# Performance work log

Hardware: AMD Instinct MI355X
Metric: run time of the kernel (lower is better)

## Reference

```python
import jax, jax.numpy as jnp
import numpy as np

B, DP, N = 8, 3, 2048
DM, K = 128, 20
C4 = DM // 4


def _gather(pts, idx):
    # pts: (b, n, c), idx: (b, n, k) -> (b, n, k, c)
    return jax.vmap(lambda p, i: p[i])(pts, idx)


def _bn(x, gamma, beta, eps=1e-5):
    # train-mode BatchNorm1d; x: (b, c, n), stats over (batch, points)
    mu = jnp.mean(x, axis=(0, 2), keepdims=True)
    var = jnp.var(x, axis=(0, 2), keepdims=True)
    return gamma[None, :, None] * (x - mu) * jax.lax.rsqrt(var + eps) + beta[None, :, None]


def setup_inputs() -> dict:
    key = jax.random.key(0)
    ks = iter(jax.random.split(key, 32))

    def U(shape):
        s = 1.0 / np.sqrt(shape[-1])
        return jax.random.uniform(next(ks), shape, jnp.float32, -s, s)

    d = {}
    d['features'] = jax.random.normal(next(ks), (B, DP, N), jnp.float32)
    d['fc1_w'] = U((DM, DP)); d['fc1_b'] = U((DM,))
    d['fc2_w'] = U((DM, DM)); d['fc2_b'] = U((DM,))
    d['bn_g'] = jnp.ones((DM,), jnp.float32); d['bn_b'] = jnp.zeros((DM,), jnp.float32)
    d['fb1_w'] = U((DM, 2 * DP)); d['fb1_b'] = U((DM,))
    d['fb2_w'] = U((DM, DM)); d['fb2_b'] = U((DM,))
    d['fg1_w'] = U((DM, DM)); d['fg1_b'] = U((DM,))
    d['fg2_w'] = U((DM, DM)); d['fg2_b'] = U((DM,))
    d['wq'] = U((DM, DM)); d['wk'] = U((DM, DM)); d['wv'] = U((DM, DM))
    d['sa_qk_w'] = U((C4, DM))  # q_conv and k_conv share this weight
    d['sa_v_w'] = U((DM, DM)); d['sa_v_b'] = U((DM,))
    d['sa_t_w'] = U((DM, DM)); d['sa_t_b'] = U((DM,))
    d['sa_bn_g'] = jnp.ones((DM,), jnp.float32); d['sa_bn_b'] = jnp.zeros((DM,), jnp.float32)
    return d


def reference(features, fc1_w, fc1_b, fc2_w, fc2_b, bn_g, bn_b,
              fb1_w, fb1_b, fb2_w, fb2_b, fg1_w, fg1_b, fg2_w, fg2_b,
              wq, wk, wv, sa_qk_w, sa_v_w, sa_v_b, sa_t_w, sa_t_b,
              sa_bn_g, sa_bn_b):
    x = features  # (b, dp, n)
    # --- kNN: negative squared pairwise distance, top-k largest = nearest ---
    inner = -2.0 * jnp.einsum('bdn,bdm->bnm', x, x)
    xx = jnp.sum(x * x, axis=1)  # (b, n)
    pd = -xx[:, :, None] - inner - xx[:, None, :]  # (b, n, n)
    idx = jax.lax.top_k(pd, K)[1]  # (b, n, K) neighbor indices
    # --- get_graph_feature: gather neighbors, concat (nbr - ctr, ctr) ---
    xt = jnp.transpose(x, (0, 2, 1))  # (b, n, dp)
    nbr = _gather(xt, idx)  # (b, n, K, dp)
    ctr = jnp.broadcast_to(xt[:, :, None, :], nbr.shape)
    kf = jnp.concatenate([nbr - ctr, ctr], axis=-1)  # (b, n, K, 2*dp)
    # fb edge MLP
    kf = jax.nn.relu(kf @ fb1_w.T + fb1_b) @ fb2_w.T + fb2_b  # (b, n, K, DM)
    # --- point-transformer attention ---
    x1 = xt @ fc1_w.T + fc1_b  # (b, n, DM)
    q = x1 @ wq.T
    kg = _gather(x1 @ wk.T, idx)  # (b, n, K, DM)
    vg = _gather(x1 @ wv.T, idx)  # (b, n, K, DM)
    a = q[:, :, None, :] - kg + kf
    a = jax.nn.relu(a @ fg1_w.T + fg1_b) @ fg2_w.T + fg2_b  # fc_gamma
    attn = jax.nn.log_softmax(a / jnp.sqrt(jnp.float32(DM)), axis=-2)  # over K
    res = jnp.einsum('bnkf,bnkf->bnf', attn, vg + kf)  # (b, n, DM)
    res = jnp.transpose(res @ fc2_w.T + fc2_b, (0, 2, 1))  # (b, DM, n)
    res = jax.nn.relu(_bn(res, bn_g, bn_b)) + jnp.transpose(x1, (0, 2, 1))
    # --- SA_Layer: offset self-attention (q and k share weights) ---
    xqk = jnp.einsum('cd,bdn->bcn', sa_qk_w, res)  # (b, C4, n)
    energy = jnp.einsum('bcn,bcm->bnm', xqk, xqk)  # (b, n, n)
    att = jax.nn.softmax(energy, axis=-1)
    att = att / (1e-9 + jnp.sum(att, axis=1, keepdims=True))
    xv = jnp.einsum('cd,bdn->bcn', sa_v_w, res) + sa_v_b[None, :, None]
    xr = jnp.einsum('bcn,bnm->bcm', xv, att)  # x_v @ attention
    xr = jnp.einsum('cd,bdn->bcn', sa_t_w, res - xr) + sa_t_b[None, :, None]
    xr = jax.nn.relu(_bn(xr, sa_bn_g, sa_bn_b))
    out = res + xr  # (b, DM, n)
    return (jnp.transpose(out, (0, 2, 1)), attn)
```

## Files before the change

### kernel.cpp

```cpp
#include <hip/hip_runtime.h>

#define NPTS 16384
#define NB 2048
#define KNN 20

typedef __attribute__((ext_vector_type(4))) float f32x4;
typedef __attribute__((ext_vector_type(8))) short short8;

union U4S8 { uint4 q; short8 s; };
union W4   { unsigned u[4]; short8 s; };

__device__ __forceinline__ unsigned bf16_rne(float v){
    unsigned u = __float_as_uint(v);
    return (u + 0x7fffu + ((u>>16)&1u)) >> 16;
}
__device__ __forceinline__ unsigned pack_hl(float v){
    unsigned hi = bf16_rne(v);
    float r = v - __uint_as_float(hi<<16);
    unsigned lo = bf16_rne(r);
    return hi | (lo<<16);
}
__device__ __forceinline__ void split_hl(uint4 w0, uint4 w1, short8& hi, short8& lo){
    W4 h, l;
    h.u[0] = __builtin_amdgcn_perm(w0.y, w0.x, 0x05040100u);
    l.u[0] = __builtin_amdgcn_perm(w0.y, w0.x, 0x07060302u);
    h.u[1] = __builtin_amdgcn_perm(w0.w, w0.z, 0x05040100u);
    l.u[1] = __builtin_amdgcn_perm(w0.w, w0.z, 0x07060302u);
    h.u[2] = __builtin_amdgcn_perm(w1.y, w1.x, 0x05040100u);
    l.u[2] = __builtin_amdgcn_perm(w1.y, w1.x, 0x07060302u);
    h.u[3] = __builtin_amdgcn_perm(w1.w, w1.z, 0x05040100u);
    l.u[3] = __builtin_amdgcn_perm(w1.w, w1.z, 0x07060302u);
    hi = h.s; lo = l.s;
}
__device__ __forceinline__ f32x4 e3_mfma(short8 Ah, short8 Al, short8 Bh, short8 Bl){
    f32x4 acc = (f32x4){0.f,0.f,0.f,0.f};
    acc = __builtin_amdgcn_mfma_f32_16x16x32_bf16(Al, Bh, acc, 0,0,0);
    acc = __builtin_amdgcn_mfma_f32_16x16x32_bf16(Ah, Bl, acc, 0,0,0);
    acc = __builtin_amdgcn_mfma_f32_16x16x32_bf16(Ah, Bh, acc, 0,0,0);
    return acc;
}

__global__ void transpose_kernel(const float* in, float* out, int C){
    int gid = blockIdx.x*256 + threadIdx.x;
    if (gid >= 128*C) return;
    int j = gid / C, c = gid - j*C;
    out[gid] = in[c*128 + j];
}

__global__ void pack_bfrag_kernel(const float* w0, const float* w1, const float* w2, unsigned short* out){
    int gid = blockIdx.x*256 + threadIdx.x;
    if (gid >= 3*16384) return;
    int m = gid >> 14, r = gid & 16383;
    const float* W = (m==0)?w0:(m==1)?w1:w2;
    int e = r & 7, lane = (r>>3) & 63, ks = (r>>9)&3, ct = r>>11;
    int c = ct*16 + (lane&15), j = ks*32 + (lane>>4)*8 + e;
    out[gid] = (unsigned short)bf16_rne(W[c*128 + j]);
}

__global__ __launch_bounds__(256) void knn_kernel(const float* feat, int* g_idx){
    __shared__ float sx[2048], sy[2048], sz[2048];
    __shared__ int swin[32*20];
    int tid = threadIdx.x;
    int p0 = blockIdx.x * 32;
    int b = p0 >> 11;
    const float* fb = feat + b*3*2048;
    for (int i = tid; i < 2048; i += 256){ sx[i]=fb[i]; sy[i]=fb[2048+i]; sz[i]=fb[4096+i]; }
    __syncthreads();

    int chunk = tid & 7, pl = tid >> 3;
    int n = (p0 + pl) & 2047;
    double xi = sx[n], yi = sy[n], zi = sz[n];

    const double SENT = __longlong_as_double(0x7FE0000000000000ll);
    double val[20];
#pragma unroll
    for (int k=0;k<20;k++) val[k] = SENT;

    int base = chunk*256;
    for (int ii=0; ii<256; ii++){
        int i = (ii + (chunk<<2)) & 255;
        int j = base + i;
        double dx = (double)sx[j]-xi, dy = (double)sy[j]-yi, dz = (double)sz[j]-zi;
        double d2 = dx*dx + dy*dy + dz*dz;
        long long kb = ((__double_as_longlong(d2) & ~2047ll) | (long long)j) + (1ll<<61);
        double key = __longlong_as_double(kb);
#pragma unroll
        for (int s=19; s>=1; s--)
            val[s] = fmax(val[s-1], fmin(val[s], key));
        val[0] = fmin(val[0], key);
    }

    for (int kk=0; kk<20; kk++){
        double h = val[0];
        h = fmin(h, __shfl_xor(h, 1));
        h = fmin(h, __shfl_xor(h, 2));
        h = fmin(h, __shfl_xor(h, 4));
        if (val[0] == h){
            swin[pl*20 + kk] = (int)(__double_as_longlong(h) & 2047ll);
#pragma unroll
            for (int s=0;s<19;s++) val[s] = val[s+1];
            val[19] = SENT;
        }
    }
    __syncthreads();
    for (int t = tid; t < 640; t += 256)
        g_idx[p0*20 + t] = swin[t];
}

__global__ void x1_kernel(const float* feat, const float* w, const float* bias, float* x1){
    int gid = blockIdx.x*256 + threadIdx.x;
    int p = gid >> 7, c = gid & 127;
    int b = p >> 11, n = p & 2047;
    const float* fb = feat + b*6144 + n;
    float v = bias[c];
    v += w[c*3+0]*fb[0];
    v += w[c*3+1]*fb[2048];
    v += w[c*3+2]*fb[4096];
    x1[gid] = v;
}

__global__ __launch_bounds__(256) void qkv_kernel(const float* x1, const float* wqT, const float* wkT,
                                                  const float* wvT, float* q, float* k1, float* v1){
    __shared__ float sx[16][128];
    int tid = threadIdx.x;
    int p0 = blockIdx.x * 16;
    for (int t = tid; t < 2048; t += 256) sx[t>>7][t&127] = x1[p0*128 + t];
    __syncthreads();
    int cg = tid & 31, pg = tid >> 5, c0 = cg*4;
    float aq[2][4] = {{0,0,0,0},{0,0,0,0}};
    float ak[2][4] = {{0,0,0,0},{0,0,0,0}};
    float av[2][4] = {{0,0,0,0},{0,0,0,0}};
    for (int j=0;j<128;j++){
        float xa = sx[pg][j], xb = sx[pg+8][j];
        float4 wq4 = *(const float4*)&wqT[j*128 + c0];
        float4 wk4 = *(const float4*)&wkT[j*128 + c0];
        float4 wv4 = *(const float4*)&wvT[j*128 + c0];
        const float* wqp = &wq4.x; const float* wkp = &wk4.x; const float* wvp = &wv4.x;
#pragma unroll
        for (int ci=0; ci<4; ci++){
            aq[0][ci] += wqp[ci]*xa; aq[1][ci] += wqp[ci]*xb;
            ak[0][ci] += wkp[ci]*xa; ak[1][ci] += wkp[ci]*xb;
            av[0][ci] += wvp[ci]*xa; av[1][ci] += wvp[ci]*xb;
        }
    }
#pragma unroll
    for (int pp=0; pp<2; pp++){
        int p = p0 + pg + pp*8;
        *(float4*)&q [p*128 + c0] = make_float4(aq[pp][0],aq[pp][1],aq[pp][2],aq[pp][3]);
        *(float4*)&k1[p*128 + c0] = make_float4(ak[pp][0],ak[pp][1],ak[pp][2],ak[pp][3]);
        *(float4*)&v1[p*128 + c0] = make_float4(av[pp][0],av[pp][1],av[pp][2],av[pp][3]);
    }
}

__device__ __forceinline__ void stage_gemm(const unsigned* buf, const unsigned short* wb,
                                           int lane, int ct0, f32x4 acc[5][2]){
    short8 bf[2][4];
#pragma unroll
    for (int ci=0; ci<2; ci++)
#pragma unroll
    for (int ks=0; ks<4; ks++){
        U4S8 u; u.q = *(const uint4*)(wb + ((ct0+ci)*4 + ks)*512 + lane*8);
        bf[ci][ks] = u.s;
    }
#pragma unroll
    for (int rt=0; rt<5; rt++)
#pragma unroll
    for (int ci=0; ci<2; ci++)
        acc[rt][ci] = (f32x4){0.f,0.f,0.f,0.f};
    int abase = (lane&15)*132 + (lane>>4)*8;
#pragma unroll
    for (int rt=0; rt<5; rt++){
#pragma unroll
        for (int ks=0; ks<4; ks++){
            const unsigned* ap = buf + rt*16*132 + ks*32 + abase;
            uint4 w0 = *(const uint4*)ap;
            uint4 w1 = *(const uint4*)(ap+4);
            short8 hi, lo;
            split_hl(w0, w1, hi, lo);
#pragma unroll
            for (int ci=0; ci<2; ci++){
                acc[rt][ci] = __builtin_amdgcn_mfma_f32_16x16x32_bf16(hi, bf[ci][ks], acc[rt][ci], 0,0,0);
                acc[rt][ci] = __builtin_amdgcn_mfma_f32_16x16x32_bf16(lo, bf[ci][ks], acc[rt][ci], 0,0,0);
            }
        }
    }
}

__global__ __launch_bounds__(256, 3) void attn_kernel(
        const float* feat, const int* g_idx, const float* g_q, const float* g_k1, const float* g_v1,
        const unsigned short* wpk,
        const float* fb1w, const float* fb1b, const float* fb2b, const float* fg1b, const float* fg2b,
        float* g_attn, float* g_res){
    __shared__ __align__(16) unsigned buf[80*132];
    __shared__ float sh_q[512];
    __shared__ float sh_e[80*6];
    __shared__ int   sh_ix[80];
    int tid = threadIdx.x;
    int lane = tid & 63, wave = tid >> 6;
    int gp0 = blockIdx.x * 4;
    int b = gp0 >> 11;
    size_t kvbase = (size_t)b*2048*128;

    sh_q[tid]     = g_q[gp0*128 + tid];
    sh_q[tid+256] = g_q[gp0*128 + tid + 256];
    if (tid < 80){
        int r = tid;
        int nb = g_idx[gp0*20 + r];
        sh_ix[r] = nb;
        int p = (r*205) >> 12;
        int n = (gp0 & 2047) + p;
        const float* fbp = feat + b*6144;
        float cx = fbp[n], cy = fbp[2048+n], cz = fbp[4096+n];
        float nx = fbp[nb], ny = fbp[2048+nb], nz = fbp[4096+nb];
        sh_e[r*6+0] = nx-cx; sh_e[r*6+1] = ny-cy; sh_e[r*6+2] = nz-cz;
        sh_e[r*6+3] = cx;    sh_e[r*6+4] = cy;    sh_e[r*6+5] = cz;
    }
    __syncthreads();

    {
        int c = tid & 127, rh = tid >> 7;
        float w0=fb1w[c*6+0], w1=fb1w[c*6+1], w2=fb1w[c*6+2], w3=fb1w[c*6+3], w4=fb1w[c*6+4], w5=fb1w[c*6+5];
        float bb = fb1b[c];
#pragma unroll
        for (int rr=0; rr<40; rr++){
            int r = rr*2 + rh;
            const float* e = &sh_e[r*6];
            float v = bb + w0*e[0]+w1*e[1]+w2*e[2]+w3*e[3]+w4*e[4]+w5*e[5];
            buf[r*132 + c] = pack_hl(fmaxf(v, 0.f));
        }
    }
    __syncthreads();

    int ct0 = wave*2;
    int colA = ct0*16 + (lane&15);
    int colB = colA + 16;
    int quad = lane >> 4;
    f32x4 acc[5][2];

    stage_gemm(buf, wpk, lane, ct0, acc);
    {
        float bA = fb2b[colA], bB = fb2b[colB];
#pragma unroll
        for (int rt=0; rt<5; rt++)
#pragma unroll
        for (int ci=0; ci<2; ci++){
            int col = ci ? colB : colA;
            float bias = ci ? bB : bA;
#pragma unroll
            for (int reg=0; reg<4; reg++){
                int row = rt*16 + quad*4 + reg;
                float kf = acc[rt][ci][reg] + bias;
                g_attn[(size_t)(gp0*20 + row)*128 + col] = kf;
                int p = (row*205)>>12;
                int nb = sh_ix[row];
                float kg = g_k1[kvbase + (size_t)nb*128 + col];
                float ain = sh_q[p*128 + col] - kg + kf;
                acc[rt][ci][reg] = __uint_as_float(pack_hl(ain));
            }
        }
    }
    __syncthreads();
#pragma unroll
    for (int rt=0; rt<5; rt++)
#pragma unroll
    for (int ci=0; ci<2; ci++)
#pragma unroll
    for (int reg=0; reg<4; reg++){
        int row = rt*16 + quad*4 + reg;
        int col = ci ? colB : colA;
        buf[row*132 + col] = __float_as_uint(acc[rt][ci][reg]);
    }
    __syncthreads();

    stage_gemm(buf, wpk + 16384, lane, ct0, acc);
    {
        float bA = fg1b[colA], bB = fg1b[colB];
#pragma unroll
        for (int rt=0; rt<5; rt++)
#pragma unroll
        for (int ci=0; ci<2; ci++){
            float bias = ci ? bB : bA;
#pragma unroll
            for (int reg=0; reg<4; reg++)
                acc[rt][ci][reg] = __uint_as_float(pack_hl(fmaxf(acc[rt][ci][reg] + bias, 0.f)));
        }
    }
    __syncthreads();
#pragma unroll
    for (int rt=0; rt<5; rt++)
#pragma unroll
    for (int ci=0; ci<2; ci++)
#pragma unroll
    for (int reg=0; reg<4; reg++){
        int row = rt*16 + quad*4 + reg;
        int col = ci ? colB : colA;
        buf[row*132 + col] = __float_as_uint(acc[rt][ci][reg]);
    }
    __syncthreads();

    stage_gemm(buf, wpk + 32768, lane, ct0, acc);
    {
        float bA = fg2b[colA], bB = fg2b[colB];
#pragma unroll
        for (int rt=0; rt<5; rt++)
#pragma unroll
        for (int ci=0; ci<2; ci++){
            float bias = ci ? bB : bA;
#pragma unroll
            for (int reg=0; reg<4; reg++)
                acc[rt][ci][reg] += bias;
        }
    }
    __syncthreads();
#pragma unroll
    for (int rt=0; rt<5; rt++)
#pragma unroll
    for (int ci=0; ci<2; ci++)
#pragma unroll
    for (int reg=0; reg<4; reg++){
        int row = rt*16 + quad*4 + reg;
        int col = ci ? colB : colA;
        buf[row*132 + col] = __float_as_uint(acc[rt][ci][reg]);
    }
    __syncthreads();

#pragma unroll
    for (int w=0; w<2; w++){
        int wk = tid + 256*w;
        int p = wk >> 7, c = wk & 127;
        float s[20];
        float m = -3e38f;
#pragma unroll
        for (int k=0;k<20;k++){
            s[k] = __uint_as_float(buf[(p*20+k)*132 + c]) * 0.08838834764831845f;
            m = fmaxf(m, s[k]);
        }
        float sum = 0.f;
#pragma unroll
        for (int k=0;k<20;k++) sum += expf(s[k] - m);
        float L = m + logf(sum);
        float* op = g_attn + (size_t)(gp0+p)*20*128 + c;
        float res = 0.f;
#pragma unroll
        for (int k=0;k<20;k++){
            float at = s[k] - L;
            float kf = op[k*128];
            int nb = sh_ix[p*20+k];
            float vv = g_v1[kvbase + (size_t)nb*128 + c];
            res += at * (vv + kf);
            op[k*128] = at;
        }
        g_res[(gp0+p)*128 + c] = res;
    }
}

__global__ __launch_bounds__(256) void lin_kernel(const float* X, const float* WT, const float* bias, float* Y){
    __shared__ float sx[16][128];
    int tid = threadIdx.x;
    int p0 = blockIdx.x * 16;
    for (int t = tid; t < 2048; t += 256) sx[t>>7][t&127] = X[p0*128 + t];
    __syncthreads();
    int cg = tid & 31, pg = tid >> 5, c0 = cg*4;
    float a[2][4] = {{0,0,0,0},{0,0,0,0}};
    for (int j=0;j<128;j++){
        float xa = sx[pg][j], xb = sx[pg+8][j];
        float4 w4 = *(const float4*)&WT[j*128 + c0];
        const float* wp = &w4.x;
#pragma unroll
        for (int ci=0;ci<4;ci++){ a[0][ci] += wp[ci]*xa; a[1][ci] += wp[ci]*xb; }
    }
    float4 bv = *(const float4*)&bias[c0];
    const float* bp = &bv.x;
#pragma unroll
    for (int pp=0;pp<2;pp++){
        int p = p0 + pg + pp*8;
        *(float4*)&Y[p*128+c0] = make_float4(a[pp][0]+bp[0], a[pp][1]+bp[1], a[pp][2]+bp[2], a[pp][3]+bp[3]);
    }
}

__global__ __launch_bounds__(256) void l6_kernel(const float* Xa, const float* Xb, const float* WT,
                                                 const float* bias, float* Y){
    __shared__ float sx[16][128];
    int tid = threadIdx.x;
    int p0 = blockIdx.x * 16;
    for (int t = tid; t < 2048; t += 256) sx[t>>7][t&127] = Xa[p0*128 + t] - Xb[p0*128 + t];
    __syncthreads();
    int cg = tid & 31, pg = tid >> 5, c0 = cg*4;
    float a[2][4] = {{0,0,0,0},{0,0,0,0}};
    for (int j=0;j<128;j++){
        float xa = sx[pg][j], xb = sx[pg+8][j];
        float4 w4 = *(const float4*)&WT[j*128 + c0];
        const float* wp = &w4.x;
#pragma unroll
        for (int ci=0;ci<4;ci++){ a[0][ci] += wp[ci]*xa; a[1][ci] += wp[ci]*xb; }
    }
    float4 bv = *(const float4*)&bias[c0];
    const float* bp = &bv.x;
#pragma unroll
    for (int pp=0;pp<2;pp++){
        int p = p0 + pg + pp*8;
        *(float4*)&Y[p*128+c0] = make_float4(a[pp][0]+bp[0], a[pp][1]+bp[1], a[pp][2]+bp[2], a[pp][3]+bp[3]);
    }
}

__global__ __launch_bounds__(256) void l5_kernel(const float* X, const float* WvT, const float* vb,
                                                 const float* WqkT, unsigned* xvt_pk, unsigned* xqk_pk){
    __shared__ float sx[16][128];
    int tid = threadIdx.x;
    int p0 = blockIdx.x * 16;
    for (int t = tid; t < 2048; t += 256) sx[t>>7][t&127] = X[p0*128 + t];
    __syncthreads();
    int cg = tid & 31, pg = tid >> 5, c0 = cg*4;
    {
        float a[2][4] = {{0,0,0,0},{0,0,0,0}};
        for (int j=0;j<128;j++){
            float xa = sx[pg][j], xb = sx[pg+8][j];
            float4 w4 = *(const float4*)&WvT[j*128 + c0];
            const float* wp = &w4.x;
#pragma unroll
            for (int ci=0;ci<4;ci++){ a[0][ci] += wp[ci]*xa; a[1][ci] += wp[ci]*xb; }
        }
        float4 bv = *(const float4*)&vb[c0];
        const float* bp = &bv.x;
#pragma unroll
        for (int pp=0;pp<2;pp++){
            int p = p0 + pg + pp*8;
            int bb = p >> 11, n = p & 2047;
            unsigned* dst = xvt_pk + ((size_t)(bb*64 + (n>>5)))*4096 + (n&31);
#pragma unroll
            for (int ci=0;ci<4;ci++) dst[(c0+ci)*32] = pack_hl(a[pp][ci] + bp[ci]);
        }
    }
    if (cg < 8){
        int cq = cg*4;
        float a[2][4] = {{0,0,0,0},{0,0,0,0}};
        for (int j=0;j<128;j++){
            float xa = sx[pg][j], xb = sx[pg+8][j];
            float4 w4 = *(const float4*)&WqkT[j*32 + cq];
            const float* wp = &w4.x;
#pragma unroll
            for (int ci=0;ci<4;ci++){ a[0][ci] += wp[ci]*xa; a[1][ci] += wp[ci]*xb; }
        }
#pragma unroll
        for (int pp=0;pp<2;pp++){
            int p = p0 + pg + pp*8;
            uint4 w;
            w.x = pack_hl(a[pp][0]); w.y = pack_hl(a[pp][1]);
            w.z = pack_hl(a[pp][2]); w.w = pack_hl(a[pp][3]);
            *(uint4*)&xqk_pk[p*32 + cq] = w;
        }
    }
}

__global__ void bn_stats_kernel(const float* X, float* sums){
    int tid = threadIdx.x;
    int c = tid & 127, half = tid >> 7;
    int r0 = blockIdx.x*128 + half*64;
    float s = 0.f, sq = 0.f;
    for (int r = r0; r < r0+64; r++){
        float v = X[r*128 + c];
        s += v; sq += v*v;
    }
    atomicAdd(&sums[c], s);
    atomicAdd(&sums[128+c], sq);
}

__global__ void bn1_apply_kernel(const float* res2, const float* x1, const float* sums,
                                 const float* g, const float* beta, float* sres){
    int gid = blockIdx.x*256 + threadIdx.x;
    int c = gid & 127;
    float mu = sums[c] * (1.0f/16384.f);
    float var = sums[128+c] * (1.0f/16384.f) - mu*mu;
    float inv = 1.0f / sqrtf(var + 1e-5f);
    float y = g[c]*(res2[gid]-mu)*inv + beta[c];
    sres[gid] = fmaxf(y, 0.f) + x1[gid];
}

__global__ void final_kernel(const float* sres, const float* xr2, const float* sums,
                             const float* g, const float* beta, float* out0){
    int gid = blockIdx.x*256 + threadIdx.x;
    int c = gid & 127;
    float mu = sums[c] * (1.0f/16384.f);
    float var = sums[128+c] * (1.0f/16384.f) - mu*mu;
    float inv = 1.0f / sqrtf(var + 1e-5f);
    float y = g[c]*(xr2[gid]-mu)*inv + beta[c];
    out0[gid] = sres[gid] + fmaxf(y, 0.f);
}

__global__ __launch_bounds__(256) void sa_stats_kernel(const unsigned* xqk_pk, float* rm, float* irs){
    int tid = threadIdx.x;
    int lane = tid & 63, wave = tid >> 6;
    int b = blockIdx.x >> 5;
    int i0 = (blockIdx.x & 31) * 64 + wave*16;
    const unsigned* qb = xqk_pk + (size_t)b*2048*32;
    int quad = lane >> 4, l15 = lane & 15;
    const unsigned* ap = qb + (i0 + l15)*32 + quad*8;
    uint4 a0 = *(const uint4*)ap, a1 = *(const uint4*)(ap+4);
    short8 Ah, Al; split_hl(a0, a1, Ah, Al);

    float m[4] = {-3e38f,-3e38f,-3e38f,-3e38f};
    for (int jt=0; jt<128; jt++){
        const unsigned* bp = qb + (jt*16 + l15)*32 + quad*8;
        uint4 b0 = *(const uint4*)bp, b1 = *(const uint4*)(bp+4);
        short8 Bh, Bl; split_hl(b0,b1,Bh,Bl);
        f32x4 e = (f32x4){0.f,0.f,0.f,0.f};
        e = __builtin_amdgcn_mfma_f32_16x16x32_bf16(Ah, Bh, e, 0,0,0);
#pragma unroll
        for (int r=0;r<4;r++) m[r] = fmaxf(m[r], e[r]);
    }
#pragma unroll
    for (int mk=1; mk<16; mk<<=1)
#pragma unroll
        for (int r=0;r<4;r++) m[r] = fmaxf(m[r], __shfl_xor(m[r], mk));

    float s[4] = {0.f,0.f,0.f,0.f};
    for (int jt=0; jt<128; jt++){
        const unsigned* bp = qb + (jt*16 + l15)*32 + quad*8;
        uint4 b0 = *(const uint4*)bp, b1 = *(const uint4*)(bp+4);
        short8 Bh, Bl; split_hl(b0,b1,Bh,Bl);
        f32x4 e = e3_mfma(Ah,Al,Bh,Bl);
#pragma unroll
        for (int r=0;r<4;r++) s[r] += expf(e[r]-m[r]);
    }
#pragma unroll
    for (int mk=1; mk<16; mk<<=1)
#pragma unroll
        for (int r=0;r<4;r++) s[r] += __shfl_xor(s[r], mk);
    if (l15 == 0){
#pragma unroll
        for (int r=0;r<4;r++){
            int row = i0 + quad*4 + r;
            rm[b*2048+row]  = m[r];
            irs[b*2048+row] = 1.0f/s[r];
        }
    }
}

#define SXV_STR 36
#define ATT_STR 36
#define NSPLIT 4
__global__ __launch_bounds__(256) void sa_xr_part_kernel(const unsigned* xqk_pk, const unsigned* xvt_pk,
                                                         const float* rm, const float* irs,
                                                         float* part, float* cspart){
    __shared__ __align__(16) unsigned sxv[128*SXV_STR];
    __shared__ __align__(16) unsigned attT[32*ATT_STR];
    __shared__ float scs[2][2][16];
    int tid = threadIdx.x;
    int lane = tid & 63, wave = tid >> 6;
    int quad = lane >> 4, l15 = lane & 15;
    int blk = blockIdx.x;
    int mt = blk & 63;
    int b  = (blk >> 6) & 7;
    int ns = blk >> 9;
    int m0 = mt*32;
    int rt = wave >> 1, ct = wave & 1;
    const unsigned* qb = xqk_pk + (size_t)b*2048*32;

    short8 Bmh, Bml;
    {
        const unsigned* bp = qb + (m0 + ct*16 + l15)*32 + quad*8;
        uint4 b0 = *(const uint4*)bp, b1 = *(const uint4*)(bp+4);
        split_hl(b0,b1,Bmh,Bml);
    }
    f32x4 acc[4];
#pragma unroll
    for (int cc=0;cc<4;cc++) acc[cc] = (f32x4){0.f,0.f,0.f,0.f};
    float cs_acc = 0.f;

    int ch0 = ns*16;
    for (int ci16=0; ci16<16; ci16++){
        int chunk = ch0 + ci16;
        int n0 = chunk*32;
        __syncthreads();
        const unsigned* src = xvt_pk + ((size_t)(b*64 + chunk))*4096;
#pragma unroll
        for (int it=0; it<4; it++){
            int u = tid + it*256;
            int c = u >> 3, part_ = u & 7;
            *(uint4*)&sxv[c*SXV_STR + part_*4] = *(const uint4*)(src + u*4);
        }
        const unsigned* ap = qb + (n0 + rt*16 + l15)*32 + quad*8;
        uint4 a0 = *(const uint4*)ap, a1 = *(const uint4*)(ap+4);
        short8 Ah, Al; split_hl(a0,a1,Ah,Al);
        f32x4 e = e3_mfma(Ah,Al,Bmh,Bml);
#pragma unroll
        for (int r=0;r<4;r++){
            int rowg = b*2048 + n0 + rt*16 + quad*4 + r;
            float att = expf(e[r] - rm[rowg]) * irs[rowg];
            cs_acc += att;
            attT[(ct*16+l15)*ATT_STR + rt*16 + quad*4 + r] = pack_hl(att);
        }
        __syncthreads();
        const unsigned* arp = attT + (ct*16+l15)*ATT_STR + quad*8;
        uint4 aa0 = *(const uint4*)arp, aa1 = *(const uint4*)(arp+4);
        short8 Aph, Apl; split_hl(aa0,aa1,Aph,Apl);
#pragma unroll
        for (int cc=0; cc<4; cc++){
            int c0 = (rt*4 + cc)*16;
            const unsigned* xp = &sxv[(c0 + l15)*SXV_STR + quad*8];
            uint4 x0 = *(const uint4*)xp, x1 = *(const uint4*)(xp+4);
            short8 Xh, Xl; split_hl(x0,x1,Xh,Xl);
            acc[cc] = __builtin_amdgcn_mfma_f32_16x16x32_bf16(Apl, Xh, acc[cc], 0,0,0);
            acc[cc] = __builtin_amdgcn_mfma_f32_16x16x32_bf16(Aph, Xl, acc[cc], 0,0,0);
            acc[cc] = __builtin_amdgcn_mfma_f32_16x16x32_bf16(Aph, Xh, acc[cc], 0,0,0);
        }
    }
    cs_acc += __shfl_xor(cs_acc, 16);
    cs_acc += __shfl_xor(cs_acc, 32);
    if (lane < 16) scs[ct][rt][lane] = cs_acc;
    __syncthreads();
    if (tid < 32)
        cspart[(size_t)(ns*8 + b)*2048 + m0 + tid] = scs[tid>>4][0][tid&15] + scs[tid>>4][1][tid&15];
#pragma unroll
    for (int cc=0; cc<4; cc++){
        int c0 = (rt*4 + cc)*16;
#pragma unroll
        for (int r=0;r<4;r++){
            int mloc = ct*16 + quad*4 + r;
            part[((size_t)(ns*8 + b)*2048 + m0 + mloc)*128 + c0 + l15] = acc[cc][r];
        }
    }
}

__global__ void sa_combine_kernel(const float* part, const float* cspart, float* xr){
    int gid = blockIdx.x*256 + threadIdx.x;
    int bm = gid >> 7;
    float cs = cspart[bm] + cspart[bm+16384] + cspart[bm+2*16384] + cspart[bm+3*16384];
    float v  = part[gid] + part[gid+2097152] + part[gid+2*2097152] + part[gid+3*2097152];
    xr[gid] = v * (1.0f/(1e-9f + cs));
}

extern "C" void kernel_launch(void* const* d_in, const int* in_sizes, int n_in,
                              void* d_out, int out_size, void* d_ws, size_t ws_size,
                              hipStream_t stream){
    (void)in_sizes; (void)n_in; (void)out_size; (void)ws_size;
    const float* feat = (const float*)d_in[0];
    const float* fc1w = (const float*)d_in[1];  const float* fc1b = (const float*)d_in[2];
    const float* fc2w = (const float*)d_in[3];  const float* fc2b = (const float*)d_in[4];
    const float* bng  = (const float*)d_in[5];  const float* bnb  = (const float*)d_in[6];
    const float* fb1w = (const float*)d_in[7];  const float* fb1b = (const float*)d_in[8];
    const float* fb2w = (const float*)d_in[9];  const float* fb2b = (const float*)d_in[10];
    const float* fg1w = (const float*)d_in[11]; const float* fg1b = (const float*)d_in[12];
    const float* fg2w = (const float*)d_in[13]; const float* fg2b = (const float*)d_in[14];
    const float* wq   = (const float*)d_in[15]; const float* wk   = (const float*)d_in[16];
    const float* wv   = (const float*)d_in[17];
    const float* saqk = (const float*)d_in[18];
    const float* savw = (const float*)d_in[19]; const float* savb = (const float*)d_in[20];
    const float* satw = (const float*)d_in[21]; const float* satb = (const float*)d_in[22];
    const float* sabng= (const float*)d_in[23]; const float* sabnb= (const float*)d_in[24];

    float* out0 = (float*)d_out;
    float* out1 = out0 + 2097152;

    char* ws = (char*)d_ws;
    size_t off = 0;
    auto A = [&](size_t bytes)->char*{
        char* r = ws + off;
        off = (off + bytes + 255) & ~(size_t)255;
        return r;
    };
    const size_t PBUF = (size_t)NPTS*128*4;
    int*      g_idx  = (int*)A((size_t)NPTS*KNN*4);
    float*    g_x1   = (float*)A(PBUF);
    float*    g_q    = (float*)A(PBUF);
    float*    g_k1   = (float*)A(PBUF);
    float*    g_v1   = (float*)A(PBUF);
    float*    g_res  = (float*)A(PBUF);
    float*    g_res2 = (float*)A(PBUF);
    float*    g_sres = (float*)A(PBUF);
    float*    g_xr   = (float*)A(PBUF);
    float*    g_xr2  = (float*)A(PBUF);
    unsigned* g_xvt_pk = (unsigned*)A((size_t)NPTS*128*4);
    unsigned* g_xqk_pk = (unsigned*)A((size_t)NPTS*32*4);
    float*    g_rm   = (float*)A((size_t)NPTS*4);
    float*    g_rs   = (float*)A((size_t)NPTS*4);
    float*    g_stats= (float*)A((size_t)512*4);
    unsigned short* g_wpk = (unsigned short*)A((size_t)3*16384*2);
    float*    g_wqT  = (float*)A(65536);
    float*    g_wkT  = (float*)A(65536);
    float*    g_wvT  = (float*)A(65536);
    float*    g_fc2T = (float*)A(65536);
    float*    g_savT = (float*)A(65536);
    float*    g_satT = (float*)A(65536);
    float*    g_sqkT = (float*)A(16384);

    float* bn1s = g_stats;
    float* bn2s = g_stats + 256;

    float* g_part   = g_q;
    float* g_cspart = g_res2;

    hipMemsetAsync(g_stats, 0, (size_t)512*4, stream);

    pack_bfrag_kernel<<<192, 256, 0, stream>>>(fb2w, fg1w, fg2w, g_wpk);
    transpose_kernel<<<64, 256, 0, stream>>>(wq,   g_wqT, 128);
    transpose_kernel<<<64, 256, 0, stream>>>(wk,   g_wkT, 128);
    transpose_kernel<<<64, 256, 0, stream>>>(wv,   g_wvT, 128);
    transpose_kernel<<<64, 256, 0, stream>>>(fc2w, g_fc2T, 128);
    transpose_kernel<<<64, 256, 0, stream>>>(savw, g_savT, 128);
    transpose_kernel<<<64, 256, 0, stream>>>(satw, g_satT, 128);
    transpose_kernel<<<16, 256, 0, stream>>>(saqk, g_sqkT, 32);

    knn_kernel<<<512, 256, 0, stream>>>(feat, g_idx);
    x1_kernel<<<8192, 256, 0, stream>>>(feat, fc1w, fc1b, g_x1);
    qkv_kernel<<<1024, 256, 0, stream>>>(g_x1, g_wqT, g_wkT, g_wvT, g_q, g_k1, g_v1);
    attn_kernel<<<4096, 256, 0, stream>>>(feat, g_idx, g_q, g_k1, g_v1, g_wpk,
                                          fb1w, fb1b, fb2b, fg1b, fg2b, out1, g_res);
    lin_kernel<<<1024, 256, 0, stream>>>(g_res, g_fc2T, fc2b, g_res2);
    bn_stats_kernel<<<128, 256, 0, stream>>>(g_res2, bn1s);
    bn1_apply_kernel<<<8192, 256, 0, stream>>>(g_res2, g_x1, bn1s, bng, bnb, g_sres);
    l5_kernel<<<1024, 256, 0, stream>>>(g_sres, g_savT, savb, g_sqkT, g_xvt_pk, g_xqk_pk);
    sa_stats_kernel<<<256, 256, 0, stream>>>(g_xqk_pk, g_rm, g_rs);
    sa_xr_part_kernel<<<512*NSPLIT, 256, 0, stream>>>(g_xqk_pk, g_xvt_pk, g_rm, g_rs, g_part, g_cspart);
    sa_combine_kernel<<<8192, 256, 0, stream>>>(g_part, g_cspart, g_xr);
    l6_kernel<<<1024, 256, 0, stream>>>(g_sres, g_xr, g_satT, satb, g_xr2);
    bn_stats_kernel<<<128, 256, 0, stream>>>(g_xr2, bn2s);
    final_kernel<<<8192, 256, 0, stream>>>(g_sres, g_xr2, bn2s, sabng, sabnb, out0);
}
```

Baseline: 792.6 us.

## Fuse log-softmax and value reduction into MFMA accumulator registers

The kf values stay in registers instead of being written to g_attn and read back later. The log-softmax over the K neighbors now runs directly on the second GEMM's accumulator fragments, using cross-lane shuffles to form per-point max and sum across the 80-row tile. This removes an LDS round trip, two block barriers and a global write-then-read of kf. In exchange it adds register pressure from kfr and the extra arrays, plus more complex shuffle logic for rows that straddle tile boundaries.

```diff
diff --git a/kernel.cpp b/kernel.cpp
--- a/kernel.cpp
+++ b/kernel.cpp
@@ -236,6 +236,7 @@
     int colB = colA + 16;
     int quad = lane >> 4;
     f32x4 acc[5][2];
+    float kfr[5][2][4];
 
     stage_gemm(buf, wpk, lane, ct0, acc);
     {
@@ -250,7 +251,7 @@
             for (int reg=0; reg<4; reg++){
                 int row = rt*16 + quad*4 + reg;
                 float kf = acc[rt][ci][reg] + bias;
-                g_attn[(size_t)(gp0*20 + row)*128 + col] = kf;
+                kfr[rt][ci][reg] = kf;
                 int p = (row*205)>>12;
                 int nb = sh_ix[row];
                 float kg = g_k1[kvbase + (size_t)nb*128 + col];
@@ -300,57 +301,88 @@
 
     stage_gemm(buf, wpk + 32768, lane, ct0, acc);
     {
+        const float SCALE = 0.08838834764831845f;
+        const float NEGF  = -3e38f;
         float bA = fg2b[colA], bB = fg2b[colB];
 #pragma unroll
-        for (int rt=0; rt<5; rt++)
-#pragma unroll
         for (int ci=0; ci<2; ci++){
+            int col = ci ? colB : colA;
             float bias = ci ? bB : bA;
-#pragma unroll
-            for (int reg=0; reg<4; reg++)
-                acc[rt][ci][reg] += bias;
-        }
-    }
-    __syncthreads();
-#pragma unroll
-    for (int rt=0; rt<5; rt++)
-#pragma unroll
-    for (int ci=0; ci<2; ci++)
-#pragma unroll
-    for (int reg=0; reg<4; reg++){
-        int row = rt*16 + quad*4 + reg;
-        int col = ci ? colB : colA;
-        buf[row*132 + col] = __float_as_uint(acc[rt][ci][reg]);
-    }
-    __syncthreads();
-
-#pragma unroll
-    for (int w=0; w<2; w++){
-        int wk = tid + 256*w;
-        int p = wk >> 7, c = wk & 127;
-        float s[20];
-        float m = -3e38f;
-#pragma unroll
-        for (int k=0;k<20;k++){
-            s[k] = __uint_as_float(buf[(p*20+k)*132 + c]) * 0.08838834764831845f;
-            m = fmaxf(m, s[k]);
-        }
-        float sum = 0.f;
-#pragma unroll
-        for (int k=0;k<20;k++) sum += expf(s[k] - m);
-        float L = m + logf(sum);
-        float* op = g_attn + (size_t)(gp0+p)*20*128 + c;
-        float res = 0.f;
-#pragma unroll
-        for (int k=0;k<20;k++){
-            float at = s[k] - L;
-            float kf = op[k*128];
-            int nb = sh_ix[p*20+k];
-            float vv = g_v1[kvbase + (size_t)nb*128 + c];
-            res += at * (vv + kf);
-            op[k*128] = at;
-        }
-        g_res[(gp0+p)*128 + c] = res;
+            float s[5][4], lm[5];
+#pragma unroll
+            for (int rt=0; rt<5; rt++){
+#pragma unroll
+                for (int reg=0; reg<4; reg++)
+                    s[rt][reg] = (acc[rt][ci][reg] + bias) * SCALE;
+                lm[rt] = fmaxf(fmaxf(s[rt][0], s[rt][1]), fmaxf(s[rt][2], s[rt][3]));
+            }
+            float m[4];
+#pragma unroll
+            for (int j=0; j<4; j++){
+                float c1 = (j<=quad) ? lm[j]   : NEGF;
+                float c2 = (j>=quad) ? lm[j+1] : NEGF;
+                m[j] = fmaxf(c1, c2);
+                m[j] = fmaxf(m[j], __shfl_xor(m[j], 16));
+                m[j] = fmaxf(m[j], __shfl_xor(m[j], 32));
+            }
+            float mp[5];
+            mp[0] = m[0];
+            mp[1] = (1<=quad) ? m[1] : m[0];
+            mp[2] = (2<=quad) ? m[2] : m[1];
+            mp[3] = (3<=quad) ? m[3] : m[2];
+            mp[4] = m[3];
+            float ls[5];
+#pragma unroll
+            for (int rt=0; rt<5; rt++){
+                float e0 = expf(s[rt][0] - mp[rt]);
+                float e1 = expf(s[rt][1] - mp[rt]);
+                float e2 = expf(s[rt][2] - mp[rt]);
+                float e3 = expf(s[rt][3] - mp[rt]);
+                ls[rt] = (e0 + e1) + (e2 + e3);
+            }
+            float L[4];
+#pragma unroll
+            for (int j=0; j<4; j++){
+                float c1 = (j<=quad) ? ls[j]   : 0.f;
+                float c2 = (j>=quad) ? ls[j+1] : 0.f;
+                float S = c1 + c2;
+                S += __shfl_xor(S, 16);
+                S += __shfl_xor(S, 32);
+                L[j] = m[j] + logf(S);
+            }
+            float Lp[5];
+            Lp[0] = L[0];
+            Lp[1] = (1<=quad) ? L[1] : L[0];
+            Lp[2] = (2<=quad) ? L[2] : L[1];
+            Lp[3] = (3<=quad) ? L[3] : L[2];
+            Lp[4] = L[3];
+            float pv[5];
+#pragma unroll
+            for (int rt=0; rt<5; rt++){
+                float pacc = 0.f;
+#pragma unroll
+                for (int reg=0; reg<4; reg++){
+                    int row = rt*16 + quad*4 + reg;
+                    float at = s[rt][reg] - Lp[rt];
+                    g_attn[(size_t)(gp0*20 + row)*128 + col] = at;
+                    int nb = sh_ix[row];
+                    float vv = g_v1[kvbase + (size_t)nb*128 + col];
+                    pacc += at * (vv + kfr[rt][ci][reg]);
+                }
+                pv[rt] = pacc;
+            }
+#pragma unroll
+            for (int j=0; j<4; j++){
+                float c1 = (j<=quad) ? pv[j]   : 0.f;
+                float c2 = (j>=quad) ? pv[j+1] : 0.f;
+                float P = c1 + c2;
+                P += __shfl_xor(P, 16);
+                P += __shfl_xor(P, 32);
+                pv[j] = P;
+            }
+            float rv = (quad==0) ? pv[0] : (quad==1) ? pv[1] : (quad==2) ? pv[2] : pv[3];
+            g_res[(size_t)(gp0 + quad)*128 + col] = rv;
+        }
     }
 }
 
```

Result: no change. 782.2 us (-1.3%).
